# Kernel tuning notes

Measured on AMD Instinct MI355X. Metric: run time of the kernel, lower is better.

The kernel has to match this reference:

```python
import jax, jax.numpy as jnp
from jax import lax
import numpy as np

WINDOW = 8
ENCOLEN = 128
HID = 128
INT_H = 128


def setup_inputs() -> dict:
    key = jax.random.key(0)
    ks = jax.random.split(key, 16)
    s = 0.05
    B, T = 512, 256
    return {
        "input_X": jax.random.normal(ks[0], (B, T, 7), jnp.float32),
        "W_ih": jax.random.normal(ks[1], (4 * HID, 5), jnp.float32) * s,
        "W_hh": jax.random.normal(ks[2], (4 * HID, HID), jnp.float32) * s,
        "b_ih": jax.random.normal(ks[3], (4 * HID,), jnp.float32) * s,
        "b_hh": jax.random.normal(ks[4], (4 * HID,), jnp.float32) * s,
        "fc1_w": jax.random.normal(ks[5], (HID, HID), jnp.float32) * s,
        "fc1_b": jax.random.normal(ks[6], (HID,), jnp.float32) * s,
        "fc2_w": jax.random.normal(ks[7], (1, HID), jnp.float32) * s,
        "fc2_b": jax.random.normal(ks[8], (1,), jnp.float32) * s,
        "int1_w": jax.random.normal(ks[9], (INT_H, 3), jnp.float32) * s,
        "int1_b": jax.random.normal(ks[10], (INT_H,), jnp.float32) * s,
        "int3_w": jax.random.normal(ks[11], (1, INT_H), jnp.float32) * s,
        "int3_b": jax.random.normal(ks[12], (1,), jnp.float32) * s,
        "scale_w": jax.random.normal(ks[13], (1, 1), jnp.float32) * s,
        "zone_w": jax.random.normal(ks[14], (1, 1), jnp.float32) * s,
    }


def _forward(input_X, W_ih, W_hh, b_ih, b_hh, fc1_w, fc1_b, fc2_w, fc2_b,
             int1_w, int1_b, int3_w, int3_b, scale_w, zone_w):
    B, T, _ = input_X.shape
    w = WINDOW
    T0 = input_X[:, :, 0:1]      # zone temperature
    Ext_X = input_X[:, :, 1:5]   # cols [1,2,3,4]
    Int_X = input_X[:, :, 3:6]   # cols [3,4,5]
    HVAC_X = input_X[:, :, 6:7]  # col [6]

    def lstm_chunk(h, c, xs):  # xs: [B, w, 5]
        def step(carry, x_t):
            h, c = carry
            g = x_t @ W_ih.T + b_ih + h @ W_hh.T + b_hh
            gi, gf, gg, go = jnp.split(g, 4, axis=-1)  # torch gate order i,f,g,o
            c = jax.nn.sigmoid(gf) * c + jax.nn.sigmoid(gi) * jnp.tanh(gg)
            h = jax.nn.sigmoid(go) * jnp.tanh(c)
            return (h, c), None
        (h, c), _ = lax.scan(step, (h, c), jnp.swapaxes(xs, 0, 1))
        return h, c  # final h == lstm_out[:, -1, :]

    def ext_module(h, c, xs):
        h, c = lstm_chunk(h, c, xs)
        o = jax.nn.relu(h @ fc1_w.T + fc1_b)
        return o @ fc2_w.T + fc2_b, h, c  # [B,1]

    # internal module is pointwise per timestep -> vectorize over all T
    # (note: FC2 in the torch module is defined but unused; faithful skip)
    int_all = jax.nn.sigmoid(
        jax.nn.relu(Int_X @ int1_w.T + int1_b) @ int3_w.T + int3_b
    ) @ scale_w.T  # [B,T,1]

    TOut = jnp.zeros((B, T, 1), input_X.dtype).at[:, :w].set(T0[:, :w])
    h = jnp.ones((B, HID), input_X.dtype)
    c = jnp.ones((B, HID), input_X.dtype)
    E = T0[:, w:w + 1, :]  # [B,1,1]

    def enc_step(carry, i):
        TOut, h, c, E = carry
        ratio = i.astype(input_X.dtype) / ENCOLEN
        TOut = lax.dynamic_update_slice(TOut, E, (0, i, 0))
        s = i - w + 1
        Tin = lax.dynamic_slice(T0, (0, s, 0), (B, w, 1))
        TOsl = lax.dynamic_slice(TOut, (0, s, 0), (B, w, 1))
        Exsl = lax.dynamic_slice(Ext_X, (0, s, 0), (B, w, 4))
        embed = jnp.concatenate([Tin * ratio + TOsl * (1.0 - ratio), Exsl], axis=2)
        ext, h, c = ext_module(h, c, embed)
        hv = lax.dynamic_slice(HVAC_X, (0, i, 0), (B, 1, 1))[:, 0]
        it = lax.dynamic_slice(int_all, (0, i, 0), (B, 1, 1))[:, 0]
        total = ext + hv + it  # [B,1]
        T0i = lax.dynamic_slice(T0, (0, i, 0), (B, 1, 1))
        E = ratio * T0i + (1.0 - ratio) * E + (total @ zone_w.T)[:, None, :]
        return (TOut, h, c, E), ext

    (TOut, h, c, E), ext_enc = lax.scan(enc_step, (TOut, h, c, E), jnp.arange(w, ENCOLEN))

    def dec_step(carry, i):
        TOut, h, c, E = carry
        TOut = lax.dynamic_update_slice(TOut, E, (0, i, 0))
        s = i - w + 1
        TOsl = lax.dynamic_slice(TOut, (0, s, 0), (B, w, 1))
        Exsl = lax.dynamic_slice(Ext_X, (0, s, 0), (B, w, 4))
        embed = jnp.concatenate([TOsl, Exsl], axis=2)
        ext, h, c = ext_module(h, c, embed)
        hv = lax.dynamic_slice(HVAC_X, (0, i, 0), (B, 1, 1))[:, 0]
        it = lax.dynamic_slice(int_all, (0, i, 0), (B, 1, 1))[:, 0]
        total = ext + hv + it
        E = (total @ zone_w.T)[:, None, :] + E
        return (TOut, h, c, E), ext

    (TOut, h, c, E), ext_dec = lax.scan(dec_step, (TOut, h, c, E), jnp.arange(ENCOLEN, T))

    Ext_list = jnp.zeros((B, T, 1), input_X.dtype)
    Ext_list = Ext_list.at[:, w:ENCOLEN].set(jnp.swapaxes(ext_enc, 0, 1))
    Ext_list = Ext_list.at[:, ENCOLEN:].set(jnp.swapaxes(ext_dec, 0, 1))
    Int_list = jnp.zeros((B, T, 1), input_X.dtype).at[:, w:].set(int_all[:, w:])
    HVAC_list = HVAC_X  # torch fills HVAC_list with HVAC_X at every step
    return TOut, HVAC_list, (Ext_list, Int_list)


def reference(input_X, W_ih, W_hh, b_ih, b_hh, fc1_w, fc1_b, fc2_w, fc2_b,
              int1_w, int1_b, int3_w, int3_b, scale_w, zone_w):
    return _forward(input_X, W_ih, W_hh, b_ih, b_hh, fc1_w, fc1_b, fc2_w, fc2_b,
                    int1_w, int1_b, int3_w, int3_b, scale_w, zone_w)
```

## Files before the change

### kernel.cpp

```cpp
#include <hip/hip_runtime.h>

#define BT   (512*256)
#define HB0b 192
#define HB1b 320
#define HLENb 448
#define LOG2E 1.44269504088896f

using short8  = __attribute__((ext_vector_type(8))) short;
using floatx4 = __attribute__((ext_vector_type(4))) float;
using int4v   = __attribute__((ext_vector_type(4))) int;
using ushort4v= __attribute__((ext_vector_type(4))) unsigned short;

__device__ inline unsigned short f2bf(float f){
  unsigned int u = __float_as_uint(f);
  u += 0x7FFFu + ((u >> 16) & 1u);
  return (unsigned short)(u >> 16);
}
__device__ inline float bf2f(unsigned short u){
  return __uint_as_float(((unsigned int)u) << 16);
}
__device__ inline float rcpf(float x){ return __builtin_amdgcn_rcpf(x); }
__device__ inline float ex2(float x){ return __builtin_amdgcn_exp2f(x); }

__global__ __launch_bounds__(512,1) void k_seq(
    const float* __restrict__ in,
    const float* __restrict__ Wih,  const float* __restrict__ Whh,
    const float* __restrict__ bih,  const float* __restrict__ bhh,
    const float* __restrict__ fc1w, const float* __restrict__ fc1b,
    const float* __restrict__ fc2w, const float* __restrict__ fc2b,
    const float* __restrict__ i1w,  const float* __restrict__ i1b,
    const float* __restrict__ i3w,  const float* __restrict__ i3b,
    const float* __restrict__ scw,  const float* __restrict__ zonew,
    float* __restrict__ out)
{
  __shared__ __align__(16) signed char hbuf[2][HLENb];
  __shared__ __align__(16) float scratch[640];
  __shared__ __align__(8)  unsigned short toutl[512];
  __shared__ __align__(8)  unsigned short extl[512];
  __shared__ __align__(16) unsigned short exl[2048];
  __shared__ float t0l[512];
  __shared__ float hvitl[512];
  __shared__ __align__(16) float parts[16];

  const int tid = threadIdx.x;
  const int wv  = tid >> 6;
  const int ln  = tid & 63;
  const int l15 = ln & 15;
  const int quad= ln >> 4;
  const int bb  = blockIdx.x;

  {
    int b=tid>>8, tt=tid&255;
    const float* row = in + (2*bb+b)*1792 + tt*7;
    t0l[tid] = row[0];
    exl[tid*4+0]=f2bf(row[1]); exl[tid*4+1]=f2bf(row[2]);
    exl[tid*4+2]=f2bf(row[3]); exl[tid*4+3]=f2bf(row[4]);
  }
  for(int p=tid; p<2*HLENb; p+=512) ((signed char*)hbuf)[p]=0;
  if(tid<16) toutl[(tid>>3)*256+(tid&7)] = f2bf(in[(2*bb+(tid>>3))*1792+(tid&7)*7]);
  float* lw4 = scratch;
  float* l3  = scratch + 512;
  if(tid<128){
    lw4[tid*4+0]=i1w[tid*3+0]; lw4[tid*4+1]=i1w[tid*3+1];
    lw4[tid*4+2]=i1w[tid*3+2]; lw4[tid*4+3]=i1b[tid];
    l3[tid]=i3w[tid];
  }
  __syncthreads();
  if(tid<256) hbuf[0][((tid>>7)? HB1b:HB0b) + (tid&127)] = 127;

  {
    const float b30=i3b[0], sc0=scw[0];
    int b=tid>>8, t=tid&255;
    const float* row = in + (2*bb+b)*1792 + t*7;
    float x0=row[3],x1=row[4],x2=row[5], acc=0.f;
    #pragma unroll 8
    for(int j=0;j<128;j++){
      float r=fmaxf(lw4[j*4]*x0+lw4[j*4+1]*x1+lw4[j*4+2]*x2+lw4[j*4+3],0.f);
      acc += r*l3[j];
    }
    float v = rcpf(1.f+__expf(-(acc+b30)))*sc0;
    float itv = (t<8)?0.f:v;
    int gb = 2*bb+b;
    hvitl[tid] = row[6] + itv;
    out[3*BT+gb*256+t]=itv;
    out[BT+gb*256+t]=row[6];
    if(t<8){ out[gb*256+t]=row[0]; out[2*BT+gb*256+t]=0.f; }
  }

  int4v wq[4][2];
  float dq[4];
  short8 xfr[4];
  float  bsum[4];
  #pragma unroll
  for(int g=0;g<4;g++){
    int n = 128*g + 16*wv + l15;
    bsum[g] = (bih[n]+bhh[n])*LOG2E;
    const float* wr = Whh + n*128;
    float mx = 1e-20f;
    for(int j=0;j<128;j++) mx = fmaxf(mx, fabsf(wr[j]));
    float qs = 127.f/mx;
    dq[g] = mx * (LOG2E/16129.f);
    #pragma unroll
    for(int c=0;c<2;c++){
      int4v v4;
      #pragma unroll
      for(int d=0;d<4;d++){
        int pk=0;
        #pragma unroll
        for(int bq=0;bq<4;bq++){
          int kk = c*64 + quad*16 + d*4 + bq;
          int q = __float2int_rn(wr[kk]*qs);
          pk |= (q & 255) << (8*bq);
        }
        v4[d]=pk;
      }
      wq[g][c]=v4;
    }
    short8 f;
    #pragma unroll
    for(int j=0;j<8;j++){ int kk=quad*8+j; f[j]=(short)f2bf(kk<5?Wih[n*5+kk]*LOG2E:0.f); }
    xfr[g]=f;
  }
  int4v fq[2]; float dqf;
  {
    int n2 = 16*wv + l15;
    const float* fr = fc1w + n2*128;
    float mx = 1e-20f;
    for(int j=0;j<128;j++) mx = fmaxf(mx, fabsf(fr[j]));
    float qs = 127.f/mx;
    dqf = mx * (1.f/16129.f);
    #pragma unroll
    for(int c=0;c<2;c++){
      int4v v4;
      #pragma unroll
      for(int d=0;d<4;d++){
        int pk=0;
        #pragma unroll
        for(int bq=0;bq<4;bq++){
          int kk = c*64 + quad*16 + d*4 + bq;
          int q = __float2int_rn(fr[kk]*qs);
          pk |= (q & 255) << (8*bq);
        }
        v4[d]=pk;
      }
      fq[c]=v4;
    }
  }

  const int  u     = 16*wv + l15;
  const int  bm    = quad & 1;
  const int  arow  = ((l15&3)==0) ? (((l15>>2)&1)? HB1b : HB0b) : 0;
  const int  aoff  = arow + quad*16;
  const int  hwoff = (bm? HB1b:HB0b) + u;
  const int  bpa0  = ((quad&1)<<7) | (l15<<2);
  const int  bpa1  = bpa0 + 64;
  const float fb    = fc1b[u];
  const float fcw_u = fc2w[u];
  const float fc2b0 = fc2b[0];
  const float zwv   = zonew[0];
  const floatx4 ZV  = {0.f,0.f,0.f,0.f};
  const int4v   ZI  = {0,0,0,0};
  const short8  Z8  = 0;
  float E0 = in[(2*bb)*1792 + 56];
  float E1 = in[(2*bb+1)*1792 + 56];
  float c0 = 1.f;
  __syncthreads();

  #pragma unroll 1
  for(int i=8;i<256;i++){
    if(i>8){
      floatx4 pa=*(const floatx4*)&parts[0];
      floatx4 pb=*(const floatx4*)&parts[4];
      floatx4 pc=*(const floatx4*)&parts[8];
      floatx4 pd=*(const floatx4*)&parts[12];
      float ext0=((pa[0]+pa[1])+(pa[2]+pa[3]))+((pb[0]+pb[1])+(pb[2]+pb[3]))+fc2b0;
      float ext1=((pc[0]+pc[1])+(pc[2]+pc[3]))+((pd[0]+pd[1])+(pd[2]+pd[3]))+fc2b0;
      int ip = i-1;
      float tot0 = ext0 + hvitl[ip];
      float tot1 = ext1 + hvitl[256+ip];
      if(ip<128){
        float ratio=(float)ip*0.0078125f;
        E0 = ratio*t0l[ip]     + (1.f-ratio)*E0 + tot0*zwv;
        E1 = ratio*t0l[256+ip] + (1.f-ratio)*E1 + tot1*zwv;
      } else {
        E0 += tot0*zwv;
        E1 += tot1*zwv;
      }
      if(tid==0){ extl[ip]=f2bf(ext0); extl[256+ip]=f2bf(ext1); }
    }
    if(tid==0){ toutl[i]=f2bf(E0); toutl[256+i]=f2bf(E1); }
    float xv[8][4];
    {
      short8 ea = Z8;
      if(quad==0){
        int bE=l15>>3, kk=l15&7, p=i-7+kk;
        float tos = (p==i) ? (bE? E1:E0) : bf2f(toutl[bE*256+p]);
        float tmix;
        if(i<128){
          float ratio=(float)i*0.0078125f;
          tmix = t0l[bE*256+p]*ratio + tos*(1.f-ratio);
        } else tmix = tos;
        ea[0]=(short)f2bf(tmix);
        ushort4v e4 = *(const ushort4v*)&exl[(bE*256+p)*4];
        ea[1]=(short)e4[0]; ea[2]=(short)e4[1];
        ea[3]=(short)e4[2]; ea[4]=(short)e4[3];
      }
      #pragma unroll
      for(int g=0;g<4;g++){
        floatx4 z=__builtin_amdgcn_mfma_f32_16x16x32_bf16(ea, xfr[g], ZV,0,0,0);
        #pragma unroll
        for(int r=0;r<4;r++){
          int zi = __float_as_int(z[r]+bsum[g]);
          xv[r][g]   = __int_as_float(__builtin_amdgcn_ds_bpermute(bpa0, zi));
          xv[r+4][g] = __int_as_float(__builtin_amdgcn_ds_bpermute(bpa1, zi));
        }
      }
    }

    #pragma unroll
    for(int k=0;k<8;k++){
      float xv0=xv[k][0];
      float xv1=xv[k][1];
      float xv2=xv[k][2];
      float xv3=xv[k][3];
      const signed char* hb = &hbuf[k&1][0];
      int4v a0 = *(const int4v*)(hb + aoff);
      int4v a1 = *(const int4v*)(hb + aoff + 64);
      int4v acc[4];
      #pragma unroll
      for(int g=0;g<4;g++){
        int4v z = __builtin_amdgcn_mfma_i32_16x16x64_i8(a0, wq[g][0], ZI,0,0,0);
        z = __builtin_amdgcn_mfma_i32_16x16x64_i8(a1, wq[g][1], z,0,0,0);
        acc[g]=z;
      }
      float gi=fmaf((float)acc[0][0],dq[0],xv0);
      float gf=fmaf((float)acc[1][0],dq[1],xv1);
      float gg=fmaf((float)acc[2][0],dq[2],xv2);
      float go=fmaf((float)acc[3][0],dq[3],xv3);
      float ef =ex2(-gf);
      float egi=ex2(-gi);
      float egg=ex2(-2.f*gg);
      float sf = rcpf(1.f+ef);
      float itn=(1.f-egg)*rcpf((1.f+egi)*(1.f+egg));
      c0 = sf*c0 + itn;
      float ego=ex2(-go);
      float ec =ex2(-2.8853900818f*c0);
      float hv2=(1.f-ec)*rcpf((1.f+ego)*(1.f+ec));
      int q = __float2int_rn(hv2*127.f);
      hbuf[(k+1)&1][hwoff] = (signed char)q;
      __syncthreads();
    }

    {
      const signed char* hb = &hbuf[0][0];
      int4v a0 = *(const int4v*)(hb + aoff);
      int4v a1 = *(const int4v*)(hb + aoff + 64);
      int4v z = __builtin_amdgcn_mfma_i32_16x16x64_i8(a0, fq[0], ZI,0,0,0);
      z = __builtin_amdgcn_mfma_i32_16x16x64_i8(a1, fq[1], z,0,0,0);
      float fv = (float)z[0]*dqf + fb;
      float pv = fmaxf(fv,0.f)*fcw_u;
      pv += __shfl_xor(pv, 1, 64);
      pv += __shfl_xor(pv, 2, 64);
      pv += __shfl_xor(pv, 4, 64);
      pv += __shfl_xor(pv, 8, 64);
      if(ln==0)       parts[wv]   = pv;
      else if(ln==16) parts[8+wv] = pv;
    }
    __syncthreads();
  }

  if(tid==0){
    float ext0 = ((parts[0]+parts[1])+(parts[2]+parts[3]))
               + ((parts[4]+parts[5])+(parts[6]+parts[7])) + fc2b0;
    float ext1 = ((parts[8]+parts[9])+(parts[10]+parts[11]))
               + ((parts[12]+parts[13])+(parts[14]+parts[15])) + fc2b0;
    extl[255]=f2bf(ext0); extl[511]=f2bf(ext1);
  }
  __syncthreads();

  for(int p=tid; p<496; p+=512){
    int b = (p>=248) ? 1 : 0;
    int i2 = p - b*248 + 8;
    int gb = 2*bb + b;
    out[gb*256+i2]      = bf2f(toutl[b*256+i2]);
    out[2*BT+gb*256+i2] = bf2f(extl[b*256+i2]);
  }
}

extern "C" void kernel_launch(void* const* d_in, const int* in_sizes, int n_in,
                              void* d_out, int out_size, void* d_ws, size_t ws_size,
                              hipStream_t stream)
{
  const float* in   = (const float*)d_in[0];
  const float* Wih  = (const float*)d_in[1];
  const float* Whh  = (const float*)d_in[2];
  const float* bih  = (const float*)d_in[3];
  const float* bhh  = (const float*)d_in[4];
  const float* fc1w = (const float*)d_in[5];
  const float* fc1b = (const float*)d_in[6];
  const float* fc2w = (const float*)d_in[7];
  const float* fc2b = (const float*)d_in[8];
  const float* i1w  = (const float*)d_in[9];
  const float* i1b  = (const float*)d_in[10];
  const float* i3w  = (const float*)d_in[11];
  const float* i3b  = (const float*)d_in[12];
  const float* scw  = (const float*)d_in[13];
  const float* zw   = (const float*)d_in[14];
  float* out = (float*)d_out;

  k_seq<<<dim3(256), dim3(512), 0, stream>>>(in, Wih, Whh, bih, bhh,
                                             fc1w, fc1b, fc2w, fc2b,
                                             i1w, i1b, i3w, i3b, scw, zw, out);
}
```

Measured before the change: 971.2 us.

## Precompute next-step input projection early, patch newest-timestep term with exact E

The input-projection MFMA for step i+1 is now issued at the end of step i, before the barrier. The one term that depends on the not-yet-known E value (the newest timestep, kk==7) is left out of that early pass. Once E is known it is added back as a scalar FMA using the first column of W_ih, scaled by (1-ratio). This takes the input-projection MFMA and bpermute latency off the serial critical path after the ext reduction. The price is slightly different rounding, because the E term is added in fp32 rather than bf16, and more register pressure from keeping xv live across iterations.

```diff
diff --git a/kernel.cpp b/kernel.cpp
--- a/kernel.cpp
+++ b/kernel.cpp
@@ -91,10 +91,12 @@
   float dq[4];
   short8 xfr[4];
   float  bsum[4];
+  float  wihc[4];
   #pragma unroll
   for(int g=0;g<4;g++){
     int n = 128*g + 16*wv + l15;
     bsum[g] = (bih[n]+bhh[n])*LOG2E;
+    wihc[g] = Wih[n*5]*LOG2E;
     const float* wr = Whh + n*128;
     float mx = 1e-20f;
     for(int j=0;j<128;j++) mx = fmaxf(mx, fabsf(wr[j]));
@@ -164,7 +166,45 @@
   float E0 = in[(2*bb)*1792 + 56];
   float E1 = in[(2*bb+1)*1792 + 56];
   float c0 = 1.f;
+  float xv[8][4];
+
+  auto bulk = [&](int it, bool exact7) {
+    short8 ea = Z8;
+    if(quad==0){
+      int bE=l15>>3, kk=l15&7, p=it-7+kk;
+      bool lt = (it<128);
+      float ratio=(float)it*0.0078125f;
+      float tmix;
+      if(kk==7){
+        if(exact7){
+          float tos = bE? E1:E0;
+          tmix = lt ? t0l[bE*256+it]*ratio + tos*(1.f-ratio) : tos;
+        } else {
+          tmix = lt ? t0l[bE*256+it]*ratio : 0.f;
+        }
+      } else {
+        float tos = bf2f(toutl[bE*256+p]);
+        tmix = lt ? t0l[bE*256+p]*ratio + tos*(1.f-ratio) : tos;
+      }
+      ea[0]=(short)f2bf(tmix);
+      ushort4v e4 = *(const ushort4v*)&exl[(bE*256+p)*4];
+      ea[1]=(short)e4[0]; ea[2]=(short)e4[1];
+      ea[3]=(short)e4[2]; ea[4]=(short)e4[3];
+    }
+    #pragma unroll
+    for(int g=0;g<4;g++){
+      floatx4 z=__builtin_amdgcn_mfma_f32_16x16x32_bf16(ea, xfr[g], ZV,0,0,0);
+      #pragma unroll
+      for(int r=0;r<4;r++){
+        int zi = __float_as_int(z[r]+bsum[g]);
+        xv[r][g]   = __int_as_float(__builtin_amdgcn_ds_bpermute(bpa0, zi));
+        xv[r+4][g] = __int_as_float(__builtin_amdgcn_ds_bpermute(bpa1, zi));
+      }
+    }
+  };
+
   __syncthreads();
+  bulk(8, true);
 
   #pragma unroll 1
   for(int i=8;i<256;i++){
@@ -187,35 +227,12 @@
         E1 += tot1*zwv;
       }
       if(tid==0){ extl[ip]=f2bf(ext0); extl[256+ip]=f2bf(ext1); }
+      float kap = (i<128) ? (1.f-(float)i*0.0078125f) : 1.f;
+      float ce  = kap * (bm ? E1 : E0);
+      #pragma unroll
+      for(int g=0;g<4;g++) xv[7][g] = fmaf(ce, wihc[g], xv[7][g]);
     }
     if(tid==0){ toutl[i]=f2bf(E0); toutl[256+i]=f2bf(E1); }
-    float xv[8][4];
-    {
-      short8 ea = Z8;
-      if(quad==0){
-        int bE=l15>>3, kk=l15&7, p=i-7+kk;
-        float tos = (p==i) ? (bE? E1:E0) : bf2f(toutl[bE*256+p]);
-        float tmix;
-        if(i<128){
-          float ratio=(float)i*0.0078125f;
-          tmix = t0l[bE*256+p]*ratio + tos*(1.f-ratio);
-        } else tmix = tos;
-        ea[0]=(short)f2bf(tmix);
-        ushort4v e4 = *(const ushort4v*)&exl[(bE*256+p)*4];
-        ea[1]=(short)e4[0]; ea[2]=(short)e4[1];
-        ea[3]=(short)e4[2]; ea[4]=(short)e4[3];
-      }
-      #pragma unroll
-      for(int g=0;g<4;g++){
-        floatx4 z=__builtin_amdgcn_mfma_f32_16x16x32_bf16(ea, xfr[g], ZV,0,0,0);
-        #pragma unroll
-        for(int r=0;r<4;r++){
-          int zi = __float_as_int(z[r]+bsum[g]);
-          xv[r][g]   = __int_as_float(__builtin_amdgcn_ds_bpermute(bpa0, zi));
-          xv[r+4][g] = __int_as_float(__builtin_amdgcn_ds_bpermute(bpa1, zi));
-        }
-      }
-    }
 
     #pragma unroll
     for(int k=0;k<8;k++){
@@ -266,6 +283,7 @@
       if(ln==0)       parts[wv]   = pv;
       else if(ln==16) parts[8+wv] = pv;
     }
+    if(i<255) bulk(i+1, false);
     __syncthreads();
   }
 
```

Measured after the change: 1.111 ms. 14.3% more time.
